# Kernel optimization log

Hardware: AMD Instinct MI355X
Metric: run time of the kernel (lower is better)

## Reference

```python
import jax, jax.numpy as jnp
import numpy as np

ALPHA = 0.2  # LeakyReLU negative slope used throughout
NEG = -9e15


def _leaky(x, a=ALPHA):
    return jnp.where(x >= 0, x, a * x)


def _gat_layer(h, adj, W, a, concat):
    # h: [N, Fin], W: [Fin, Fout], a: [2*Fout, 1]
    Wh = h @ W                                   # [N, Fout]
    d = W.shape[-1]
    e = _leaky(Wh @ a[:d] + (Wh @ a[d:]).T)      # [N, N]
    att = jax.nn.softmax(jnp.where(adj > 0, e, NEG), axis=1)
    out = att @ Wh                               # [N, Fout]
    return jax.nn.elu(out) if concat else out


def setup_inputs() -> dict:
    key = jax.random.key(0)
    ks = jax.random.split(key, 24)
    N, F, H, D1, O1 = 4096, 512, 4, 256, 64
    x = jax.random.normal(ks[0], (N, F), dtype=jnp.float32)
    adj = jax.random.bernoulli(ks[1], 0.02, (N, N))
    adj = (adj | adj.T | jnp.eye(N, dtype=bool)).astype(jnp.float32)
    observation = jax.random.randint(ks[2], (1, N), 0, 2, dtype=jnp.int32)
    s_mat = jax.random.uniform(ks[3], (N, N), dtype=jnp.float32)
    theta = jax.random.uniform(ks[4], (1, F), dtype=jnp.float32)
    g = lambda k, s, sc: (jax.random.normal(k, s, dtype=jnp.float32) * sc)
    return {
        'x': x, 'adj': adj, 'observation': observation, 's_mat': s_mat,
        'theta': theta,
        'Wh0': g(ks[5], (H, F, D1), 0.05), 'ah0': g(ks[6], (H, 2 * D1, 1), 0.05),
        'Wh1': g(ks[7], (H, D1, D1), 0.05), 'ah1': g(ks[8], (H, 2 * D1, 1), 0.05),
        'Wo0': g(ks[9], (H * D1, O1), 0.05), 'ao0': g(ks[10], (2 * O1, 1), 0.05),
        'Wo1': g(ks[11], (O1, 1), 0.2), 'ao1': g(ks[12], (2, 1), 0.2),
        'dW': g(ks[13], (2, 10), 0.5), 'dW0': g(ks[14], (1, 10), 0.5),
        'dW1': g(ks[15], (10, 20), 0.5), 'dW01': g(ks[16], (1, 20), 0.5),
        'dW2': g(ks[17], (20, 10), 0.5), 'dW02': g(ks[18], (1, 10), 0.5),
        'dV': g(ks[19], (10, 1), 0.5), 'dV0': g(ks[20], (1, 1), 0.5),
    }


def reference(x, adj, observation, s_mat, theta, Wh0, ah0, Wh1, ah1,
              Wo0, ao0, Wo1, ao1, dW, dW0, dW1, dW01, dW2, dW02, dV, dV0):
    # mergeState: add theta to rows in the seed set (observation[0] == 1)
    seed = (observation[0] == 1).astype(x.dtype)[:, None]  # [N,1]
    h_in = x + seed * theta

    # multi-head 2-layer attention stacks (concat=True -> elu inside)
    def head(W0, a0, W1, a1):
        h = _gat_layer(h_in, adj, W0, a0, True)
        return _gat_layer(h, adj, W1, a1, True)

    hh = jax.vmap(head)(Wh0, ah0, Wh1, ah1)                 # [H, N, D1]
    hcat = jnp.transpose(hh, (1, 0, 2)).reshape(h_in.shape[0], -1)  # [N, H*D1]

    # output attention stack (concat=False), then elu (GAT.forward)
    h = _gat_layer(hcat, adj, Wo0, ao0, False)
    h = _gat_layer(h, adj, Wo1, ao1, False)
    h_ = jax.nn.elu(h)                                      # [N, 1]

    # GAT_degree v2: degreeNN over [h_, degree]
    d_v = s_mat.sum(axis=1, keepdims=True)                  # [N, 1]
    x_ = jnp.concatenate([h_, d_v], axis=1)                 # [N, 2]
    h0 = _leaky(x_ @ dW + dW0)
    h1 = _leaky(h0 @ dW1 + dW01)
    h2 = _leaky(h1 @ dW2 + dW02)
    return _leaky(h2 @ dV + dV0)                            # [N, 1]
```

## Files before the change

kernel.cpp:

```cpp
#include <hip/hip_runtime.h>
#include <hip/hip_bf16.h>
#include <hip/hip_fp16.h>
#include <math.h>

#define MAXDEG 512

typedef short v8s __attribute__((ext_vector_type(8)));
typedef float v4f __attribute__((ext_vector_type(4)));
typedef _Float16 h2 __attribute__((ext_vector_type(2)));

__device__ __forceinline__ float blockReduceSum(float v) {
    __shared__ float sh[8];
    int lane = threadIdx.x & 63, w = threadIdx.x >> 6;
    for (int o = 32; o > 0; o >>= 1) v += __shfl_down(v, o);
    __syncthreads();
    if (lane == 0) sh[w] = v;
    __syncthreads();
    if (w == 0) {
        int nw = (blockDim.x + 63) >> 6;
        v = (lane < nw) ? sh[lane] : 0.f;
        for (int o = 4; o > 0; o >>= 1) v += __shfl_down(v, o);
        if (lane == 0) sh[0] = v;
    }
    __syncthreads();
    return sh[0];
}

__device__ __forceinline__ float blockReduceMax(float v) {
    __shared__ float sh[8];
    int lane = threadIdx.x & 63, w = threadIdx.x >> 6;
    for (int o = 32; o > 0; o >>= 1) v = fmaxf(v, __shfl_down(v, o));
    __syncthreads();
    if (lane == 0) sh[w] = v;
    __syncthreads();
    if (w == 0) {
        int nw = (blockDim.x + 63) >> 6;
        v = (lane < nw) ? sh[lane] : -3.4e38f;
        for (int o = 4; o > 0; o >>= 1) v = fmaxf(v, __shfl_down(v, o));
        if (lane == 0) sh[0] = v;
    }
    __syncthreads();
    return sh[0];
}

__device__ __forceinline__ float leaky(float x) { return x >= 0.f ? x : 0.2f * x; }


__global__ void fused_pre(const float* __restrict__ adj, const float* __restrict__ s,
                          int* __restrict__ colIdx, int* __restrict__ deg,
                          float* __restrict__ dv,
                          const float* __restrict__ x, const int* __restrict__ obs,
                          const float* __restrict__ theta,
                          const float* __restrict__ Wh0, const float* __restrict__ Wh1,
                          const float* __restrict__ Wo0,
                          __half* __restrict__ hin, __half* __restrict__ Wh0t,
                          __half* __restrict__ Wh1t, __half* __restrict__ Wo0t,
                          float* __restrict__ elerZ, int elerN, int N) {
    const int tid = threadIdx.x;
    if (blockIdx.x < 4096) {
        int row = blockIdx.x;
        __shared__ int cnt;
        if (tid == 0) cnt = 0;
        __syncthreads();
        const float4* ar = (const float4*)(adj + (size_t)row * N);
        const float4* sr = (const float4*)(s + (size_t)row * N);
        int* outp = colIdx + (size_t)row * MAXDEG;
        float psum = 0.f;
        const int n4 = N >> 2;
        for (int j4 = tid; j4 < n4; j4 += blockDim.x) {
            float4 a4 = ar[j4];
            float4 s4 = sr[j4];
            psum += (s4.x + s4.y) + (s4.z + s4.w);
            int jb = j4 << 2;
            if (a4.x > 0.f) { int p = atomicAdd(&cnt, 1); if (p < MAXDEG) outp[p] = jb; }
            if (a4.y > 0.f) { int p = atomicAdd(&cnt, 1); if (p < MAXDEG) outp[p] = jb + 1; }
            if (a4.z > 0.f) { int p = atomicAdd(&cnt, 1); if (p < MAXDEG) outp[p] = jb + 2; }
            if (a4.w > 0.f) { int p = atomicAdd(&cnt, 1); if (p < MAXDEG) outp[p] = jb + 3; }
        }
        psum = blockReduceSum(psum);
        __syncthreads();
        if (tid == 0) {
            deg[row] = cnt < MAXDEG ? cnt : MAXDEG;
            dv[row] = psum;
        }
        return;
    }
    int bb = blockIdx.x - 4096;
    if (bb < 1024) {
        int i8 = bb * 256 + tid;
        int n = i8 >> 6;
        int f = (i8 & 63) * 8;
        float4 a = *(const float4*)(x + (size_t)i8 * 8);
        float4 b = *(const float4*)(x + (size_t)i8 * 8 + 4);
        if (obs[n] == 1) {
            float4 ta = *(const float4*)(theta + f);
            float4 tb = *(const float4*)(theta + f + 4);
            a.x += ta.x; a.y += ta.y; a.z += ta.z; a.w += ta.w;
            b.x += tb.x; b.y += tb.y; b.z += tb.z; b.w += tb.w;
        }
        __half hv[8];
        hv[0] = __float2half(a.x); hv[1] = __float2half(a.y);
        hv[2] = __float2half(a.z); hv[3] = __float2half(a.w);
        hv[4] = __float2half(b.x); hv[5] = __float2half(b.y);
        hv[6] = __float2half(b.z); hv[7] = __float2half(b.w);
        *(uint4*)(hin + (size_t)i8 * 8) = *(const uint4*)hv;
        return;
    }
    bb -= 1024;
    if (bb < 72) {
        int i = bb * 256 + tid;
        *(float4*)(elerZ + (size_t)i * 4) = make_float4(0.f, 0.f, 0.f, 0.f);
        return;
    }
    int t = bb - 72;
    const float* src;
    __half* dst;
    int srcStride, dstStride;
    if (t < 128) {
        int b = t >> 5, tt = t & 31, kt = tt >> 2, mt = tt & 3;
        src = Wh0 + b * 131072 + (kt * 64) * 256 + mt * 64;
        dst = Wh0t + b * 131072 + (mt * 64) * 512 + kt * 64;
        srcStride = 256; dstStride = 512;
    } else if (t < 192) {
        int u = t - 128;
        int b = u >> 4, tt = u & 15, kt = tt >> 2, mt = tt & 3;
        src = Wh1 + b * 65536 + (kt * 64) * 256 + mt * 64;
        dst = Wh1t + b * 65536 + (mt * 64) * 256 + kt * 64;
        srcStride = 256; dstStride = 256;
    } else {
        int kt = t - 192;
        src = Wo0 + (kt * 64) * 64;
        dst = Wo0t + kt * 64;
        srcStride = 64; dstStride = 1024;
    }
    __shared__ float tile[64][65];
    int rr = tid >> 4;
    int cc = (tid & 15) * 4;
    #pragma unroll
    for (int sI = 0; sI < 4; sI++) {
        float4 v = *(const float4*)(src + (size_t)(rr + sI * 16) * srcStride + cc);
        tile[rr + sI * 16][cc]     = v.x;
        tile[rr + sI * 16][cc + 1] = v.y;
        tile[rr + sI * 16][cc + 2] = v.z;
        tile[rr + sI * 16][cc + 3] = v.w;
    }
    __syncthreads();
    int mr = tid >> 2;
    int kc = (tid & 3) * 16;
    #pragma unroll
    for (int g = 0; g < 2; g++) {
        v8s v;
        #pragma unroll
        for (int e = 0; e < 8; e++)
            v[e] = (short)__half_as_ushort(__float2half(tile[kc + g * 8 + e][mr]));
        *(v8s*)(dst + (size_t)mr * dstStride + kc + g * 8) = v;
    }
}

__global__ __launch_bounds__(256) void gemm_mfma64x128(
    const __half* __restrict__ A, const __half* __restrict__ Bt,
    __half* __restrict__ C, int N, int K, int M,
    size_t sA, size_t sB, size_t sC,
    const float* __restrict__ aVec, size_t aStride,
    float* __restrict__ el, float* __restrict__ er) {
    int b = blockIdx.z;
    const unsigned short* Ag = (const unsigned short*)(A + (size_t)b * sA);
    const unsigned short* Bg = (const unsigned short*)(Bt + (size_t)b * sB);
    __half* Cg = C + (size_t)b * sC;
    const float* av = aVec + (size_t)b * aStride;

    __shared__ __align__(16) unsigned short As[64][40];
    __shared__ __align__(16) unsigned short Bs[128][40];

    const int tid = threadIdx.x;
    const int wave = tid >> 6, lane = tid & 63;
    const int row0 = blockIdx.y * 64, col0 = blockIdx.x * 128;
    const int lr = tid >> 2;
    const int lo = (tid & 3) * 8;
    const int m = lane & 15, quad = lane >> 4;

    v4f acc[8];
    #pragma unroll
    for (int c = 0; c < 8; c++) acc[c] = (v4f)(0.f);

    for (int k0 = 0; k0 < K; k0 += 32) {
        *(int4*)(&As[lr][lo]) =
            *(const int4*)(Ag + (size_t)(row0 + lr) * K + k0 + lo);
        *(int4*)(&Bs[lr][lo]) =
            *(const int4*)(Bg + (size_t)(col0 + lr) * K + k0 + lo);
        *(int4*)(&Bs[lr + 64][lo]) =
            *(const int4*)(Bg + (size_t)(col0 + 64 + lr) * K + k0 + lo);
        __syncthreads();
        v8s af = *(const v8s*)(&As[wave * 16 + m][quad * 8]);
        #pragma unroll
        for (int c = 0; c < 8; c++) {
            v8s bfv = *(const v8s*)(&Bs[c * 16 + m][quad * 8]);
            acc[c] = __builtin_amdgcn_mfma_f32_16x16x32_f16(af, bfv, acc[c], 0, 0, 0);
        }
        __syncthreads();
    }
    #pragma unroll
    for (int c = 0; c < 8; c++)
        #pragma unroll
        for (int r = 0; r < 4; r++) {
            int row = row0 + wave * 16 + quad * 4 + r;
            int col = col0 + c * 16 + m;
            Cg[(size_t)row * M + col] = __float2half(acc[c][r]);
        }
    float ael[8], aer[8];
    #pragma unroll
    for (int c = 0; c < 8; c++) {
        ael[c] = av[col0 + c * 16 + m];
        aer[c] = av[M + col0 + c * 16 + m];
    }
    #pragma unroll
    for (int r = 0; r < 4; r++) {
        float pel = 0.f, per_ = 0.f;
        #pragma unroll
        for (int c = 0; c < 8; c++) {
            pel += acc[c][r] * ael[c];
            per_ += acc[c][r] * aer[c];
        }
        #pragma unroll
        for (int off = 1; off < 16; off <<= 1) {
            pel += __shfl_xor(pel, off);
            per_ += __shfl_xor(per_, off);
        }
        if (m == 0) {
            int row = row0 + wave * 16 + quad * 4 + r;
            atomicAdd(&el[(size_t)b * N + row], pel);
            atomicAdd(&er[(size_t)b * N + row], per_);
        }
    }
}

__global__ __launch_bounds__(256) void gemm_mfma64(
    const __half* __restrict__ A, const __half* __restrict__ Bt,
    __half* __restrict__ C, int N, int K, int M,
    size_t sA, size_t sB, size_t sC,
    const float* __restrict__ aVec, size_t aStride,
    float* __restrict__ el, float* __restrict__ er) {
    int b = blockIdx.z;
    const unsigned short* Ag = (const unsigned short*)(A + (size_t)b * sA);
    const unsigned short* Bg = (const unsigned short*)(Bt + (size_t)b * sB);
    __half* Cg = C + (size_t)b * sC;
    const float* av = aVec + (size_t)b * aStride;

    __shared__ __align__(16) unsigned short As[64][40];
    __shared__ __align__(16) unsigned short Bs[64][40];

    const int tid = threadIdx.x;
    const int wave = tid >> 6, lane = tid & 63;
    const int row0 = blockIdx.y * 64, col0 = blockIdx.x * 64;
    const int sRow = tid >> 2;
    const int sOff = (tid & 3) * 8;
    const int m = lane & 15, quad = lane >> 4;

    v4f acc[4];
    #pragma unroll
    for (int c = 0; c < 4; c++) acc[c] = (v4f)(0.f);

    for (int k0 = 0; k0 < K; k0 += 32) {
        *(int4*)(&As[sRow][sOff]) =
            *(const int4*)(Ag + (size_t)(row0 + sRow) * K + k0 + sOff);
        *(int4*)(&Bs[sRow][sOff]) =
            *(const int4*)(Bg + (size_t)(col0 + sRow) * K + k0 + sOff);
        __syncthreads();
        v8s af = *(const v8s*)(&As[wave * 16 + m][quad * 8]);
        #pragma unroll
        for (int c = 0; c < 4; c++) {
            v8s bfv = *(const v8s*)(&Bs[c * 16 + m][quad * 8]);
            acc[c] = __builtin_amdgcn_mfma_f32_16x16x32_f16(af, bfv, acc[c], 0, 0, 0);
        }
        __syncthreads();
    }
    #pragma unroll
    for (int c = 0; c < 4; c++)
        #pragma unroll
        for (int r = 0; r < 4; r++) {
            int row = row0 + wave * 16 + quad * 4 + r;
            int col = col0 + c * 16 + m;
            Cg[(size_t)row * M + col] = __float2half(acc[c][r]);
        }
    float ael[4], aer[4];
    #pragma unroll
    for (int c = 0; c < 4; c++) {
        ael[c] = av[col0 + c * 16 + m];
        aer[c] = av[M + col0 + c * 16 + m];
    }
    #pragma unroll
    for (int r = 0; r < 4; r++) {
        float pel = 0.f, per_ = 0.f;
        #pragma unroll
        for (int c = 0; c < 4; c++) {
            pel += acc[c][r] * ael[c];
            per_ += acc[c][r] * aer[c];
        }
        #pragma unroll
        for (int off = 1; off < 16; off <<= 1) {
            pel += __shfl_xor(pel, off);
            per_ += __shfl_xor(per_, off);
        }
        if (m == 0) {
            int row = row0 + wave * 16 + quad * 4 + r;
            atomicAdd(&el[(size_t)b * N + row], pel);
            atomicAdd(&er[(size_t)b * N + row], per_);
        }
    }
}

template<int D, int ACT, int HEADS, int FUSE>
__global__ __launch_bounds__(128) void attn_vec(
    const __half* __restrict__ Wh, const float* __restrict__ el,
    const float* __restrict__ er, const int* __restrict__ colIdx,
    const int* __restrict__ deg, __half* __restrict__ out,
    int N, size_t sWh, size_t sOut, int outRowStride,
    const float* __restrict__ wo1, const float* __restrict__ ao1,
    float* __restrict__ o2wh, float* __restrict__ el4, float* __restrict__ er4) {
    constexpr int LPN = D / 8;
    constexpr int SUBS = 64 / LPN;
    constexpr int PER_WAVE = SUBS * 4;
    constexpr int STEP = PER_WAVE * 2;

    const int tid = threadIdx.x;
    const int wave = tid >> 6, lane = tid & 63;
    int b, row;
    if (HEADS == 4) {
        int xcd = blockIdx.x & 7;
        b = xcd >> 1;
        row = ((xcd & 1) << 11) + ((blockIdx.x >> 3) << 1) + wave;
    } else {
        b = 0;
        row = blockIdx.x * 2 + wave;
    }

    const __half* whb = Wh + (size_t)b * sWh;
    const float* erb = er + (size_t)b * N;
    const float eln = el[(size_t)b * N + row];
    const int dc = deg[row];
    const int dcp = (dc + STEP - 1) & ~(STEP - 1);
    const int* ci = colIdx + (size_t)row * MAXDEG;

    __shared__ __align__(16) float2 spc[2][MAXDEG];
    float2* sp = spc[wave];

    float sreg[8];
    int jreg[8];
    float mx = -3.4e38f;
    #pragma unroll
    for (int s8 = 0; s8 < 8; s8++) {
        int k = s8 * 64 + lane;
        if (k < dc) {
            int j = ci[k];
            float s = eln + erb[j];
            s = fmaxf(s, 0.2f * s);
            sreg[s8] = s;
            jreg[s8] = j * (D * 2);
            mx = fmaxf(mx, s);
        }
    }
    #pragma unroll
    for (int off = 1; off < 64; off <<= 1) mx = fmaxf(mx, __shfl_xor(mx, off));

    float l = 0.f;
    #pragma unroll
    for (int s8 = 0; s8 < 8; s8++) {
        int k = s8 * 64 + lane;
        if (k < dc) {
            float p = __expf(sreg[s8] - mx);
            l += p;
            unsigned int pu = __half_as_ushort(__float2half(p));
            sp[k] = make_float2(__int_as_float(pu | (pu << 16)),
                                __int_as_float(jreg[s8]));
        }
    }
    for (int k = dc + lane; k < dcp; k += 64)
        sp[k] = make_float2(__int_as_float(0), __int_as_float(0));
    #pragma unroll
    for (int off = 1; off < 64; off <<= 1) l += __shfl_xor(l, off);
    const float inv = 1.f / l;

    asm volatile("s_waitcnt lgkmcnt(0)" ::: "memory");

    const int sub = lane / LPN;
    const int dl = (lane % LPN) * 8;
    const char* wp = (const char*)(whb + dl);

    union HU { unsigned int u; h2 h; };
    union R4 { uint4 u; h2 h[4]; };

    h2 a0[4], a1[4], a2[4], a3[4];
    #pragma unroll
    for (int i = 0; i < 4; i++) {
        a0[i] = (h2)(_Float16)0; a1[i] = (h2)(_Float16)0;
        a2[i] = (h2)(_Float16)0; a3[i] = (h2)(_Float16)0;
    }

    for (int k = sub * 4; k < dcp; k += STEP) {
        float4 pA = *(const float4*)(&sp[k]);
        float4 pB = *(const float4*)(&sp[k + 2]);
        float4 pC = *(const float4*)(&sp[k + PER_WAVE]);
        float4 pD = *(const float4*)(&sp[k + PER_WAVE + 2]);
        R4 r0, r1, r2, r3, r4, r5, r6, r7;
        r0.u = *(const uint4*)(wp + __float_as_int(pA.y));
        r1.u = *(const uint4*)(wp + __float_as_int(pA.w));
        r2.u = *(const uint4*)(wp + __float_as_int(pB.y));
        r3.u = *(const uint4*)(wp + __float_as_int(pB.w));
        r4.u = *(const uint4*)(wp + __float_as_int(pC.y));
        r5.u = *(const uint4*)(wp + __float_as_int(pC.w));
        r6.u = *(const uint4*)(wp + __float_as_int(pD.y));
        r7.u = *(const uint4*)(wp + __float_as_int(pD.w));
        HU p0, p1, p2, p3, p4, p5, p6, p7;
        p0.u = __float_as_int(pA.x);
        p1.u = __float_as_int(pA.z);
        p2.u = __float_as_int(pB.x);
        p3.u = __float_as_int(pB.z);
        p4.u = __float_as_int(pC.x);
        p5.u = __float_as_int(pC.z);
        p6.u = __float_as_int(pD.x);
        p7.u = __float_as_int(pD.z);
        #pragma unroll
        for (int i = 0; i < 4; i++) {
            a0[i] += p0.h * r0.h[i];
            a1[i] += p2.h * r2.h[i];
            a2[i] += p4.h * r4.h[i];
            a3[i] += p6.h * r6.h[i];
        }
        #pragma unroll
        for (int i = 0; i < 4; i++) {
            a0[i] += p1.h * r1.h[i];
            a1[i] += p3.h * r3.h[i];
            a2[i] += p5.h * r5.h[i];
            a3[i] += p7.h * r7.h[i];
        }
    }
    #pragma unroll
    for (int i = 0; i < 4; i++) a0[i] += (a1[i] + (a2[i] + a3[i]));
    #pragma unroll
    for (int off = LPN; off < 64; off <<= 1)
        #pragma unroll
        for (int i = 0; i < 4; i++) {
            HU t, s;
            t.h = a0[i];
            s.u = __shfl_xor((int)t.u, off);
            a0[i] += s.h;
        }

    if (FUSE) {
        if (sub == 0) {
            float t = 0.f;
            #pragma unroll
            for (int i = 0; i < 4; i++) {
                t += (float)a0[i][0] * inv * wo1[dl + 2 * i];
                t += (float)a0[i][1] * inv * wo1[dl + 2 * i + 1];
            }
            #pragma unroll
            for (int off = 1; off < LPN; off <<= 1) t += __shfl_xor(t, off);
            if (lane == 0) {
                o2wh[row] = t;
                el4[row] = t * ao1[0];
                er4[row] = t * ao1[1];
            }
        }
        return;
    }
    if (sub == 0) {
        __half hv[8];
        #pragma unroll
        for (int i = 0; i < 4; i++) {
            float v0 = (float)a0[i][0] * inv;
            float v1 = (float)a0[i][1] * inv;
            if (ACT == 1) {
                v0 = (v0 > 0.f) ? v0 : expm1f(v0);
                v1 = (v1 > 0.f) ? v1 : expm1f(v1);
            }
            hv[2 * i]     = __float2half(v0);
            hv[2 * i + 1] = __float2half(v1);
        }
        *(uint4*)(out + (size_t)b * sOut + (size_t)row * outRowStride + dl) =
            *(const uint4*)hv;
    }
}

__global__ void attn_d1_deg(const float* __restrict__ o2wh, const float* __restrict__ el,
                            const float* __restrict__ er, const int* __restrict__ colIdx,
                            const int* __restrict__ deg, const float* __restrict__ dv,
                            const float* __restrict__ dW, const float* __restrict__ dW0,
                            const float* __restrict__ dW1, const float* __restrict__ dW01,
                            const float* __restrict__ dW2, const float* __restrict__ dW02,
                            const float* __restrict__ dV, const float* __restrict__ dV0,
                            float* __restrict__ out, int N) {
    int row = blockIdx.x, tid = threadIdx.x;
    const float eln = el[row];
    const int dc = deg[row];
    const int* ci = colIdx + (size_t)row * MAXDEG;
    __shared__ float sp[MAXDEG];
    __shared__ int sc[MAXDEG];
    float mx = -3.4e38f;
    for (int k = tid; k < dc; k += blockDim.x) {
        int j = ci[k];
        sc[k] = j;
        float s = eln + er[j];
        s = fmaxf(s, 0.2f * s);
        sp[k] = s;
        mx = fmaxf(mx, s);
    }
    mx = blockReduceMax(mx);
    float l = 0.f, acc = 0.f;
    for (int k = tid; k < dc; k += blockDim.x) {
        float p = __expf(sp[k] - mx);
        l += p;
        acc += p * o2wh[sc[k]];
    }
    l = blockReduceSum(l);
    acc = blockReduceSum(acc);
    if (tid == 0) {
        float h = acc / l;
        h = (h > 0.f) ? h : expm1f(h);
        float d = dv[row];
        float t0[10], t1[20], t2[10];
        #pragma unroll
        for (int i = 0; i < 10; i++)
            t0[i] = leaky(h * dW[i] + d * dW[10 + i] + dW0[i]);
        #pragma unroll
        for (int j = 0; j < 20; j++) {
            float s = dW01[j];
            #pragma unroll
            for (int i = 0; i < 10; i++) s += t0[i] * dW1[i * 20 + j];
            t1[j] = leaky(s);
        }
        #pragma unroll
        for (int j = 0; j < 10; j++) {
            float s = dW02[j];
            #pragma unroll
            for (int i = 0; i < 20; i++) s += t1[i] * dW2[i * 10 + j];
            t2[j] = leaky(s);
        }
        float o = dV0[0];
        #pragma unroll
        for (int i = 0; i < 10; i++) o += t2[i] * dV[i];
        out[row] = leaky(o);
    }
}

extern "C" void kernel_launch(void* const* d_in, const int* in_sizes, int n_in,
                              void* d_out, int out_size, void* d_ws, size_t ws_size,
                              hipStream_t stream) {
    const int N = 4096, F = 512, H = 4, D1 = 256, O1 = 64;
    const float* x     = (const float*)d_in[0];
    const float* adj   = (const float*)d_in[1];
    const int*   obs   = (const int*)  d_in[2];
    const float* s_mat = (const float*)d_in[3];
    const float* theta = (const float*)d_in[4];
    const float* Wh0   = (const float*)d_in[5];
    const float* ah0   = (const float*)d_in[6];
    const float* Wh1   = (const float*)d_in[7];
    const float* ah1   = (const float*)d_in[8];
    const float* Wo0   = (const float*)d_in[9];
    const float* ao0   = (const float*)d_in[10];
    const float* Wo1   = (const float*)d_in[11];
    const float* ao1   = (const float*)d_in[12];
    const float* dWp   = (const float*)d_in[13];
    const float* dW0p  = (const float*)d_in[14];
    const float* dW1p  = (const float*)d_in[15];
    const float* dW01p = (const float*)d_in[16];
    const float* dW2p  = (const float*)d_in[17];
    const float* dW02p = (const float*)d_in[18];
    const float* dVp   = (const float*)d_in[19];
    const float* dV0p  = (const float*)d_in[20];
    float* outp = (float*)d_out;

    char* ws = (char*)d_ws;
    auto alloc = [&](size_t bytes) {
        char* p = ws;
        ws += (bytes + 255) & ~(size_t)255;
        return p;
    };
    __half* hin  = (__half*)alloc((size_t)N * F * 2);
    __half* whA  = (__half*)alloc((size_t)H * N * D1 * 2);
    __half* hb   = (__half*)alloc((size_t)H * N * D1 * 2);
    __half* hcat = (__half*)alloc((size_t)N * H * D1 * 2);
    __half* o1Wh = (__half*)alloc((size_t)N * O1 * 2);
    float* o2Wh  = (float*)alloc((size_t)N * 4);
    __half* Wh0t = (__half*)alloc((size_t)H * F * D1 * 2);
    __half* Wh1t = (__half*)alloc((size_t)H * D1 * D1 * 2);
    __half* Wo0t = (__half*)alloc((size_t)H * D1 * O1 * 2);
    int elerN = 4 * H * N + 2 * N;
    float* elerZ = (float*)alloc((size_t)elerN * 4);
    float* el1 = elerZ;
    float* er1 = el1 + H * N;
    float* el2 = er1 + H * N;
    float* er2 = el2 + H * N;
    float* el3 = er2 + H * N;
    float* er3 = el3 + N;
    float* el4 = (float*)alloc((size_t)N * 4);
    float* er4 = (float*)alloc((size_t)N * 4);
    float* dv  = (float*)alloc((size_t)N * 4);
    int* colIdx = (int*)alloc((size_t)N * MAXDEG * 4);
    int* deg    = (int*)alloc((size_t)N * 4);

    {
        fused_pre<<<4096 + 1024 + 72 + 208, 256, 0, stream>>>(
            adj, s_mat, colIdx, deg, dv,
            x, obs, theta, Wh0, Wh1, Wo0, hin, Wh0t, Wh1t, Wo0t, elerZ, elerN, N);
    }

    gemm_mfma64x128<<<dim3(D1 / 128, N / 64, H), 256, 0, stream>>>(
        hin, Wh0t, whA, N, F, D1, 0, (size_t)D1 * F, (size_t)N * D1,
        ah0, (size_t)2 * D1, el1, er1);
    attn_vec<256, 1, 4, 0><<<(N * H) / 2, 128, 0, stream>>>(
        whA, el1, er1, colIdx, deg, hb,
        N, (size_t)N * D1, (size_t)N * D1, D1,
        nullptr, nullptr, nullptr, nullptr, nullptr);

    gemm_mfma64x128<<<dim3(D1 / 128, N / 64, H), 256, 0, stream>>>(
        hb, Wh1t, whA, N, D1, D1, (size_t)N * D1, (size_t)D1 * D1, (size_t)N * D1,
        ah1, (size_t)2 * D1, el2, er2);
    attn_vec<256, 1, 4, 0><<<(N * H) / 2, 128, 0, stream>>>(
        whA, el2, er2, colIdx, deg, hcat,
        N, (size_t)N * D1, (size_t)D1, H * D1,
        nullptr, nullptr, nullptr, nullptr, nullptr);

    gemm_mfma64<<<dim3(O1 / 64, N / 64, 1), 256, 0, stream>>>(
        hcat, Wo0t, o1Wh, N, H * D1, O1, 0, 0, 0,
        ao0, 0, el3, er3);
    attn_vec<64, 0, 1, 1><<<N / 2, 128, 0, stream>>>(
        o1Wh, el3, er3, colIdx, deg, nullptr,
        N, 0, 0, O1,
        Wo1, ao1, o2Wh, el4, er4);

    attn_d1_deg<<<N, 256, 0, stream>>>(o2Wh, el4, er4, colIdx, deg, dv,
        dWp, dW0p, dW1p, dW01p, dW2p, dW02p, dVp, dV0p, outp, N);
}
```

Measured before the change: 382.9 us.

## Retile head GEMM to 2x2 wave grid with K=64 steps; add 16-row output GEMM

The 64x128 head GEMM now arranges its four waves as a 2x2 grid, each computing 32x64 with register reuse of A and B fragments, and consumes 64 of K per shared-memory stage to halve the barrier count. The output-layer GEMM (M=64) is replaced by a 16-row-tile kernel so that N/16 blocks are launched instead of N/64, giving more parallelism for this narrow GEMM. The trade-off is more shared memory per block and redundant reloads of B in the new small kernel.

```diff
diff --git a/kernel.cpp b/kernel.cpp
--- a/kernel.cpp
+++ b/kernel.cpp
@@ -169,142 +169,157 @@
     __half* Cg = C + (size_t)b * sC;
     const float* av = aVec + (size_t)b * aStride;
 
-    __shared__ __align__(16) unsigned short As[64][40];
-    __shared__ __align__(16) unsigned short Bs[128][40];
+    __shared__ __align__(16) unsigned short As[64][72];
+    __shared__ __align__(16) unsigned short Bs[128][72];
 
     const int tid = threadIdx.x;
     const int wave = tid >> 6, lane = tid & 63;
+    const int wm = wave >> 1, wn = wave & 1;
     const int row0 = blockIdx.y * 64, col0 = blockIdx.x * 128;
     const int lr = tid >> 2;
-    const int lo = (tid & 3) * 8;
+    const int lo = (tid & 3) * 16;
     const int m = lane & 15, quad = lane >> 4;
 
-    v4f acc[8];
-    #pragma unroll
-    for (int c = 0; c < 8; c++) acc[c] = (v4f)(0.f);
-
-    for (int k0 = 0; k0 < K; k0 += 32) {
+    v4f acc[2][4];
+    #pragma unroll
+    for (int i = 0; i < 2; i++)
+        #pragma unroll
+        for (int c = 0; c < 4; c++) acc[i][c] = (v4f)(0.f);
+
+    for (int k0 = 0; k0 < K; k0 += 64) {
         *(int4*)(&As[lr][lo]) =
             *(const int4*)(Ag + (size_t)(row0 + lr) * K + k0 + lo);
+        *(int4*)(&As[lr][lo + 8]) =
+            *(const int4*)(Ag + (size_t)(row0 + lr) * K + k0 + lo + 8);
         *(int4*)(&Bs[lr][lo]) =
             *(const int4*)(Bg + (size_t)(col0 + lr) * K + k0 + lo);
+        *(int4*)(&Bs[lr][lo + 8]) =
+            *(const int4*)(Bg + (size_t)(col0 + lr) * K + k0 + lo + 8);
         *(int4*)(&Bs[lr + 64][lo]) =
             *(const int4*)(Bg + (size_t)(col0 + 64 + lr) * K + k0 + lo);
+        *(int4*)(&Bs[lr + 64][lo + 8]) =
+            *(const int4*)(Bg + (size_t)(col0 + 64 + lr) * K + k0 + lo + 8);
         __syncthreads();
-        v8s af = *(const v8s*)(&As[wave * 16 + m][quad * 8]);
-        #pragma unroll
-        for (int c = 0; c < 8; c++) {
-            v8s bfv = *(const v8s*)(&Bs[c * 16 + m][quad * 8]);
-            acc[c] = __builtin_amdgcn_mfma_f32_16x16x32_f16(af, bfv, acc[c], 0, 0, 0);
+        #pragma unroll
+        for (int ks = 0; ks < 2; ks++) {
+            v8s af[2], bfv[4];
+            #pragma unroll
+            for (int i = 0; i < 2; i++)
+                af[i] = *(const v8s*)(&As[wm * 32 + i * 16 + m][ks * 32 + quad * 8]);
+            #pragma unroll
+            for (int c = 0; c < 4; c++)
+                bfv[c] = *(const v8s*)(&Bs[wn * 64 + c * 16 + m][ks * 32 + quad * 8]);
+            #pragma unroll
+            for (int i = 0; i < 2; i++)
+                #pragma unroll
+                for (int c = 0; c < 4; c++)
+                    acc[i][c] = __builtin_amdgcn_mfma_f32_16x16x32_f16(
+                        af[i], bfv[c], acc[i][c], 0, 0, 0);
         }
         __syncthreads();
     }
     #pragma unroll
-    for (int c = 0; c < 8; c++)
+    for (int i = 0; i < 2; i++)
+        #pragma unroll
+        for (int c = 0; c < 4; c++)
+            #pragma unroll
+            for (int r = 0; r < 4; r++) {
+                int row = row0 + wm * 32 + i * 16 + quad * 4 + r;
+                int col = col0 + wn * 64 + c * 16 + m;
+                Cg[(size_t)row * M + col] = __float2half(acc[i][c][r]);
+            }
+    float ael[4], aer[4];
+    #pragma unroll
+    for (int c = 0; c < 4; c++) {
+        ael[c] = av[col0 + wn * 64 + c * 16 + m];
+        aer[c] = av[M + col0 + wn * 64 + c * 16 + m];
+    }
+    #pragma unroll
+    for (int i = 0; i < 2; i++)
         #pragma unroll
         for (int r = 0; r < 4; r++) {
-            int row = row0 + wave * 16 + quad * 4 + r;
-            int col = col0 + c * 16 + m;
-            Cg[(size_t)row * M + col] = __float2half(acc[c][r]);
-        }
-    float ael[8], aer[8];
-    #pragma unroll
-    for (int c = 0; c < 8; c++) {
-        ael[c] = av[col0 + c * 16 + m];
-        aer[c] = av[M + col0 + c * 16 + m];
+            float pel = 0.f, per_ = 0.f;
+            #pragma unroll
+            for (int c = 0; c < 4; c++) {
+                pel += acc[i][c][r] * ael[c];
+                per_ += acc[i][c][r] * aer[c];
+            }
+            #pragma unroll
+            for (int off = 1; off < 16; off <<= 1) {
+                pel += __shfl_xor(pel, off);
+                per_ += __shfl_xor(per_, off);
+            }
+            if (m == 0) {
+                int row = row0 + wm * 32 + i * 16 + quad * 4 + r;
+                atomicAdd(&el[(size_t)b * N + row], pel);
+                atomicAdd(&er[(size_t)b * N + row], per_);
+            }
+        }
+}
+
+__global__ __launch_bounds__(256) void gemm_mfma16(
+    const __half* __restrict__ A, const __half* __restrict__ Bt,
+    __half* __restrict__ C, int N, int K, int M,
+    const float* __restrict__ aVec,
+    float* __restrict__ el, float* __restrict__ er) {
+    const unsigned short* Ag = (const unsigned short*)A;
+    const unsigned short* Bg = (const unsigned short*)Bt;
+    __half* Cg = C;
+    const float* av = aVec;
+
+    __shared__ __align__(16) unsigned short As[16][72];
+    __shared__ __align__(16) unsigned short Bs[64][72];
+
+    const int tid = threadIdx.x;
+    const int wave = tid >> 6, lane = tid & 63;
+    const int row0 = blockIdx.y * 16;
+    const int m = lane & 15, quad = lane >> 4;
+
+    v4f acc = (v4f)(0.f);
+
+    for (int k0 = 0; k0 < K; k0 += 64) {
+        if (tid < 128) {
+            int ar = tid >> 3, ac = (tid & 7) * 8;
+            *(int4*)(&As[ar][ac]) =
+                *(const int4*)(Ag + (size_t)(row0 + ar) * K + k0 + ac);
+        }
+        {
+            int br = tid >> 2, bc = (tid & 3) * 16;
+            *(int4*)(&Bs[br][bc]) =
+                *(const int4*)(Bg + (size_t)br * K + k0 + bc);
+            *(int4*)(&Bs[br][bc + 8]) =
+                *(const int4*)(Bg + (size_t)br * K + k0 + bc + 8);
+        }
+        __syncthreads();
+        #pragma unroll
+        for (int ks = 0; ks < 2; ks++) {
+            v8s af = *(const v8s*)(&As[m][ks * 32 + quad * 8]);
+            v8s bf = *(const v8s*)(&Bs[wave * 16 + m][ks * 32 + quad * 8]);
+            acc = __builtin_amdgcn_mfma_f32_16x16x32_f16(af, bf, acc, 0, 0, 0);
+        }
+        __syncthreads();
     }
     #pragma unroll
     for (int r = 0; r < 4; r++) {
-        float pel = 0.f, per_ = 0.f;
-        #pragma unroll
-        for (int c = 0; c < 8; c++) {
-            pel += acc[c][r] * ael[c];
-            per_ += acc[c][r] * aer[c];
-        }
+        int row = row0 + quad * 4 + r;
+        int col = wave * 16 + m;
+        Cg[(size_t)row * M + col] = __float2half(acc[r]);
+    }
+    float ael = av[wave * 16 + m];
+    float aer = av[M + wave * 16 + m];
+    #pragma unroll
+    for (int r = 0; r < 4; r++) {
+        float pel = acc[r] * ael;
+        float per_ = acc[r] * aer;
         #pragma unroll
         for (int off = 1; off < 16; off <<= 1) {
             pel += __shfl_xor(pel, off);
             per_ += __shfl_xor(per_, off);
         }
         if (m == 0) {
-            int row = row0 + wave * 16 + quad * 4 + r;
-            atomicAdd(&el[(size_t)b * N + row], pel);
-            atomicAdd(&er[(size_t)b * N + row], per_);
-        }
-    }
-}
-
-__global__ __launch_bounds__(256) void gemm_mfma64(
-    const __half* __restrict__ A, const __half* __restrict__ Bt,
-    __half* __restrict__ C, int N, int K, int M,
-    size_t sA, size_t sB, size_t sC,
-    const float* __restrict__ aVec, size_t aStride,
-    float* __restrict__ el, float* __restrict__ er) {
-    int b = blockIdx.z;
-    const unsigned short* Ag = (const unsigned short*)(A + (size_t)b * sA);
-    const unsigned short* Bg = (const unsigned short*)(Bt + (size_t)b * sB);
-    __half* Cg = C + (size_t)b * sC;
-    const float* av = aVec + (size_t)b * aStride;
-
-    __shared__ __align__(16) unsigned short As[64][40];
-    __shared__ __align__(16) unsigned short Bs[64][40];
-
-    const int tid = threadIdx.x;
-    const int wave = tid >> 6, lane = tid & 63;
-    const int row0 = blockIdx.y * 64, col0 = blockIdx.x * 64;
-    const int sRow = tid >> 2;
-    const int sOff = (tid & 3) * 8;
-    const int m = lane & 15, quad = lane >> 4;
-
-    v4f acc[4];
-    #pragma unroll
-    for (int c = 0; c < 4; c++) acc[c] = (v4f)(0.f);
-
-    for (int k0 = 0; k0 < K; k0 += 32) {
-        *(int4*)(&As[sRow][sOff]) =
-            *(const int4*)(Ag + (size_t)(row0 + sRow) * K + k0 + sOff);
-        *(int4*)(&Bs[sRow][sOff]) =
-            *(const int4*)(Bg + (size_t)(col0 + sRow) * K + k0 + sOff);
-        __syncthreads();
-        v8s af = *(const v8s*)(&As[wave * 16 + m][quad * 8]);
-        #pragma unroll
-        for (int c = 0; c < 4; c++) {
-            v8s bfv = *(const v8s*)(&Bs[c * 16 + m][quad * 8]);
-            acc[c] = __builtin_amdgcn_mfma_f32_16x16x32_f16(af, bfv, acc[c], 0, 0, 0);
-        }
-        __syncthreads();
-    }
-    #pragma unroll
-    for (int c = 0; c < 4; c++)
-        #pragma unroll
-        for (int r = 0; r < 4; r++) {
-            int row = row0 + wave * 16 + quad * 4 + r;
-            int col = col0 + c * 16 + m;
-            Cg[(size_t)row * M + col] = __float2half(acc[c][r]);
-        }
-    float ael[4], aer[4];
-    #pragma unroll
-    for (int c = 0; c < 4; c++) {
-        ael[c] = av[col0 + c * 16 + m];
-        aer[c] = av[M + col0 + c * 16 + m];
-    }
-    #pragma unroll
-    for (int r = 0; r < 4; r++) {
-        float pel = 0.f, per_ = 0.f;
-        #pragma unroll
-        for (int c = 0; c < 4; c++) {
-            pel += acc[c][r] * ael[c];
-            per_ += acc[c][r] * aer[c];
-        }
-        #pragma unroll
-        for (int off = 1; off < 16; off <<= 1) {
-            pel += __shfl_xor(pel, off);
-            per_ += __shfl_xor(per_, off);
-        }
-        if (m == 0) {
-            int row = row0 + wave * 16 + quad * 4 + r;
-            atomicAdd(&el[(size_t)b * N + row], pel);
-            atomicAdd(&er[(size_t)b * N + row], per_);
+            int row = row0 + quad * 4 + r;
+            atomicAdd(&el[row], pel);
+            atomicAdd(&er[row], per_);
         }
     }
 }
@@ -621,9 +636,9 @@
         N, (size_t)N * D1, (size_t)D1, H * D1,
         nullptr, nullptr, nullptr, nullptr, nullptr);
 
-    gemm_mfma64<<<dim3(O1 / 64, N / 64, 1), 256, 0, stream>>>(
-        hcat, Wo0t, o1Wh, N, H * D1, O1, 0, 0, 0,
-        ao0, 0, el3, er3);
+    gemm_mfma16<<<dim3(1, N / 16, 1), 256, 0, stream>>>(
+        hcat, Wo0t, o1Wh, N, H * D1, O1,
+        ao0, el3, er3);
     attn_vec<64, 0, 1, 1><<<N / 2, 128, 0, stream>>>(
         o1Wh, el3, er3, colIdx, deg, nullptr,
         N, 0, 0, O1,
```

New measurement: 377.3 us. No clear change (-1.5%).
